# Performance work log

Measured on AMD Instinct MI355X. Metric: run time of the kernel, lower is better.

Reference implementation:

```python
import jax, jax.numpy as jnp
import numpy as np

N = 8192
C = 256


def setup_inputs() -> dict:
    key = jax.random.key(0)
    k_x, k_wr, k_br, k_wc, k_bc = jax.random.split(key, 5)
    scale = 1.0 / np.sqrt(C)
    return {
        "x": jax.random.normal(k_x, (N, C), dtype=jnp.float32),
        "w_reduce": jax.random.uniform(k_wr, (C, C), dtype=jnp.float32, minval=-scale, maxval=scale),
        "b_reduce": jax.random.uniform(k_br, (C,), dtype=jnp.float32, minval=-scale, maxval=scale),
        "w_contr": jax.random.uniform(k_wc, (1, C), dtype=jnp.float32, minval=-scale, maxval=scale),
        "b_contr": jax.random.uniform(k_bc, (1,), dtype=jnp.float32, minval=-scale, maxval=scale),
    }


def reference(x, w_reduce, b_reduce, w_contr, b_contr):
    # Original math: y_ij = reduce(x_i + x_j); z_ij = sigmoid(contr(y_ij));
    # out_i = mean_j y_ij * z_ij.
    # Since reduce/contr are affine, decompose without the [N,N,C] tensor:
    #   y_ij = r_i + r_j + b_reduce,        r = x @ Wr^T
    #   contr(y_ij) = s_i + s_j + c0,       s = r . wc, c0 = b_reduce . wc + bc
    n = x.shape[0]
    r = x @ w_reduce.T                                   # [N, C]
    wc = w_contr[0]                                      # [C]
    s = r @ wc                                           # [N]
    c0 = b_reduce @ wc + b_contr[0]                      # scalar
    Z = jax.nn.sigmoid(s[:, None] + s[None, :] + c0)     # [N, N] pairwise gate
    m = jnp.mean(Z, axis=1, keepdims=True)               # [N, 1]
    # mean_j (r_i + r_j + b) * z_ij = (r_i + b) * m_i + (Z @ r)_i / N
    out = (r + b_reduce) * m + (Z @ r) / n               # [N, C]
    return out
```

## Files before the change

### kernel.cpp

```cpp
#include <hip/hip_runtime.h>
#include <hip/hip_bf16.h>
#include <stdint.h>

#define NN 8192
#define CC 256
#define NSPLIT 8
#define JR (NN / NSPLIT)
#define NITER (JR / 32)

typedef float f32x4 __attribute__((ext_vector_type(4)));
typedef float f32x2 __attribute__((ext_vector_type(2)));
typedef short s16x8 __attribute__((ext_vector_type(8)));

#define LOG2E 1.4426950408889634f

#define OFF_WT  0
#define OFF_R   (OFF_WT + CC*CC)
#define OFF_S2  (OFF_R + NN*CC)
#define OFF_C0  (OFF_S2 + NN)
#define OFF_SS  (OFF_C0 + 16)
#define OFF_SP  (OFF_SS + NSPLIT*NN)
#define OFF_V   (OFF_SP + 4*NN)
#define OFF_RB  (OFF_V + (NSPLIT*NN*CC)/2)

__global__ __launch_bounds__(256) void k_prep(const float* __restrict__ w,
                                              const float* __restrict__ br,
                                              const float* __restrict__ wcv,
                                              const float* __restrict__ bc,
                                              float* __restrict__ ws) {
  int k = blockIdx.x, c = threadIdx.x;
  ws[OFF_WT + k * CC + c] = w[c * CC + k];
  if (blockIdx.x == 0 && threadIdx.x < 64) {
    int lane = threadIdx.x;
    f32x4 b4 = *(const f32x4*)&br[lane * 4];
    f32x4 w4 = *(const f32x4*)&wcv[lane * 4];
    float d = b4[0]*w4[0] + b4[1]*w4[1] + b4[2]*w4[2] + b4[3]*w4[3];
    #pragma unroll
    for (int m = 32; m >= 1; m >>= 1) d += __shfl_xor(d, m, 64);
    if (lane == 0) { ws[OFF_C0] = d + bc[0]; ws[OFF_C0 + 1] = (d + bc[0]) * LOG2E; }
  }
}

__global__ __launch_bounds__(256) void k_r(const float* __restrict__ x,
                                           const float* __restrict__ wcv,
                                           float* __restrict__ ws) {
  __shared__ float xs[64][260];
  int bi = blockIdx.x;
  int rowblk = bi >> 2, colblk = bi & 3;
  int tid = threadIdx.x;
  int i0 = rowblk * 64;
  for (int t = tid; t < 64 * 64; t += 256) {
    int rr = t >> 6, c4 = t & 63;
    *(f32x4*)&xs[rr][c4 * 4] = *(const f32x4*)&x[(i0 + rr) * CC + c4 * 4];
  }
  __syncthreads();
  int tx = tid & 15, ty = tid >> 4;
  int cbase = colblk * 64 + tx * 4;
  int r0 = ty * 4;
  float acc[4][4] = {};
  const float* wt = ws + OFF_WT;
  for (int k = 0; k < CC; k += 2) {
    f32x4 wv0 = *(const f32x4*)&wt[k * CC + cbase];
    f32x4 wv1 = *(const f32x4*)&wt[(k + 1) * CC + cbase];
    f32x2 xv[4];
    #pragma unroll
    for (int rr = 0; rr < 4; rr++) xv[rr] = *(const f32x2*)&xs[r0 + rr][k];
    #pragma unroll
    for (int rr = 0; rr < 4; rr++)
      #pragma unroll
      for (int cc = 0; cc < 4; cc++)
        acc[rr][cc] = fmaf(xv[rr][1], wv1[cc], fmaf(xv[rr][0], wv0[cc], acc[rr][cc]));
  }
  #pragma unroll
  for (int rr = 0; rr < 4; rr++) {
    f32x4 o = {acc[rr][0], acc[rr][1], acc[rr][2], acc[rr][3]};
    *(f32x4*)&ws[OFF_R + (size_t)(i0 + r0 + rr) * CC + cbase] = o;
  }
  unsigned long long* rb64 = (unsigned long long*)(ws + OFF_RB);
  int j0r = i0 + r0;
  #pragma unroll
  for (int cc = 0; cc < 4; cc++) {
    int c = cbase + cc;
    unsigned long long v = 0;
    #pragma unroll
    for (int rr = 0; rr < 4; rr++) {
      unsigned u = __float_as_uint(acc[rr][cc]);
      u = (u + 0x7fffu + ((u >> 16) & 1u)) >> 16;
      v |= (unsigned long long)u << (16 * rr);
    }
    int us = (((j0r >> 5) * 16 + (c >> 4)) * 64 + (((j0r >> 3) & 3) * 16 + (c & 15))) * 8 + (j0r & 7);
    rb64[us >> 2] = v;
  }
  f32x4 wc4 = *(const f32x4*)&wcv[cbase];
  float sd[4];
  #pragma unroll
  for (int rr = 0; rr < 4; rr++) {
    sd[rr] = acc[rr][0]*wc4[0] + acc[rr][1]*wc4[1] + acc[rr][2]*wc4[2] + acc[rr][3]*wc4[3];
    #pragma unroll
    for (int m = 1; m < 16; m <<= 1) sd[rr] += __shfl_xor(sd[rr], m, 64);
  }
  if (tx == 0) {
    #pragma unroll
    for (int rr = 0; rr < 4; rr++)
      ws[OFF_SP + colblk * NN + j0r + rr] = sd[rr];
  }
}

__global__ __launch_bounds__(256) void k_s2(float* __restrict__ ws) {
  int row = blockIdx.x * 256 + threadIdx.x;
  float s = ws[OFF_SP + row] + ws[OFF_SP + NN + row]
          + ws[OFF_SP + 2 * NN + row] + ws[OFF_SP + 3 * NN + row];
  ws[OFF_S2 + row] = s * LOG2E;
}


#define STAGE(BUF, IT) { \
  const char* gb_ = rbase + (size_t)(IT) * 16384 + w * 1024 + l * 16; \
  _Pragma("unroll") \
  for (int q_ = 0; q_ < 8; q_++) \
    __builtin_amdgcn_global_load_lds( \
      (const __attribute__((address_space(1))) void*)(gb_ + q_ * 2048), \
      (__attribute__((address_space(3))) void*)&ldsb[(BUF) * 16384 + w * 1024 + q_ * 2048 + l * 16], \
      16, 0, 0); }

#define WAITBAR0 { asm volatile("s_waitcnt vmcnt(0)" ::: "memory"); \
  __builtin_amdgcn_s_barrier(); \
  __builtin_amdgcn_sched_barrier(0); }

#define SB0 __builtin_amdgcn_sched_barrier(0);

#define SIGMOID(IT, AFA, AFB) { \
  f32x4 sj0_ = *(const f32x4*)&s2l[(IT) * 32 + g * 8]; \
  f32x4 sj1_ = *(const f32x4*)&s2l[(IT) * 32 + g * 8 + 4]; \
  _Pragma("unroll") \
  for (int t_ = 0; t_ < 8; t_++) { \
    float sj_ = (t_ < 4) ? sj0_[t_] : sj1_[t_ - 4]; \
    float eA_, eB_; \
    asm("v_exp_f32 %0, %1" : "=v"(eA_) : "v"(negaA - sj_)); \
    asm("v_exp_f32 %0, %1" : "=v"(eB_) : "v"(negaB - sj_)); \
    float zA_ = __builtin_amdgcn_rcpf(1.0f + eA_); \
    float zB_ = __builtin_amdgcn_rcpf(1.0f + eB_); \
    (AFA)[t_] = (short)(__float_as_uint(zA_) >> 16); \
    (AFB)[t_] = (short)(__float_as_uint(zB_) >> 16); } }

#define MFMA_PHASE(AFA, AFB, LP) { \
  _Pragma("unroll") \
  for (int ct_ = 0; ct_ < 16; ct_++) { \
    s16x8 bf_ = *(const s16x8*)((LP) + ct_ * 1024 + l * 16); \
    accA[ct_] = __builtin_amdgcn_mfma_f32_16x16x32_bf16(AFA, bf_, accA[ct_], 0, 0, 0); \
    accB[ct_] = __builtin_amdgcn_mfma_f32_16x16x32_bf16(AFB, bf_, accB[ct_], 0, 0, 0); } \
  acc1A = __builtin_amdgcn_mfma_f32_16x16x32_bf16(AFA, ones, acc1A, 0, 0, 0); \
  acc1B = __builtin_amdgcn_mfma_f32_16x16x32_bf16(AFB, ones, acc1B, 0, 0, 0); }

__global__ __launch_bounds__(128, 2) void k_main(float* __restrict__ ws) {
  __shared__ char ldsb[2 * 16384];
  __shared__ float s2l[1024];
  int blk = blockIdx.x;
  int rt = blk >> 3, h = blk & 7;
  int tid = threadIdx.x;
  int w = tid >> 6, l = tid & 63;
  int lr = l & 15, g = l >> 4;
  int iw = rt * 64 + w * 32;
  float c02 = ws[OFF_C0 + 1];
  float negaA = -(ws[OFF_S2 + iw + lr] + c02);
  float negaB = -(ws[OFF_S2 + iw + 16 + lr] + c02);

  const float* s2p = ws + OFF_S2 + h * JR;
  *(f32x4*)&s2l[tid * 4] = *(const f32x4*)(s2p + tid * 4);
  *(f32x4*)&s2l[(tid + 128) * 4] = *(const f32x4*)(s2p + (tid + 128) * 4);
  __syncthreads();

  f32x4 accA[16], accB[16], acc1A, acc1B;
  #pragma unroll
  for (int i = 0; i < 16; i++) { accA[i] = (f32x4)(0.f); accB[i] = (f32x4)(0.f); }
  acc1A = (f32x4)(0.f); acc1B = (f32x4)(0.f);
  s16x8 ones;
  #pragma unroll
  for (int t = 0; t < 8; t++) ones[t] = (short)0x3F80;

  const char* rbase = (const char*)(ws + OFF_RB) + (size_t)h * (JR * CC * 2);

  STAGE(0, 0);
  s16x8 afA, afB;
  #pragma unroll 1
  for (int J = 0; J < NITER; ++J) {
    WAITBAR0;
    if (J + 1 < NITER) STAGE((J + 1) & 1, J + 1);
    SB0;
    SIGMOID(J, afA, afB);
    MFMA_PHASE(afA, afB, ldsb + (J & 1) * 16384);
  }

  if (lr == 0) {
    #pragma unroll
    for (int q = 0; q < 4; q++) {
      ws[OFF_SS + h * NN + iw + g * 4 + q] = acc1A[q];
      ws[OFF_SS + h * NN + iw + 16 + g * 4 + q] = acc1B[q];
    }
  }
  unsigned short* Vb = (unsigned short*)(ws + OFF_V);
  size_t vbase = (size_t)h * (NN * CC);
  #pragma unroll
  for (int ct = 0; ct < 16; ct++) {
    #pragma unroll
    for (int q = 0; q < 4; q++) {
      unsigned uA = __float_as_uint(accA[ct][q]);
      uA = (uA + 0x7fffu + ((uA >> 16) & 1u)) >> 16;
      Vb[vbase + (size_t)(iw + g * 4 + q) * CC + ct * 16 + lr] = (unsigned short)uA;
      unsigned uB = __float_as_uint(accB[ct][q]);
      uB = (uB + 0x7fffu + ((uB >> 16) & 1u)) >> 16;
      Vb[vbase + (size_t)(iw + 16 + g * 4 + q) * CC + ct * 16 + lr] = (unsigned short)uB;
    }
  }
}

__global__ __launch_bounds__(256) void k_epi(const float* __restrict__ br,
                                             const float* __restrict__ ws,
                                             float* __restrict__ out) {
  int idx = blockIdx.x * 256 + threadIdx.x;
  int i = idx >> 5, c8 = (idx & 31) * 8;
  float S = 0.f;
  #pragma unroll
  for (int p = 0; p < NSPLIT; p++) S += ws[OFF_SS + p * NN + i];
  float m = S * (1.0f / NN);
  float v[8] = {};
  const unsigned short* Vb = (const unsigned short*)(ws + OFF_V);
  #pragma unroll
  for (int p = 0; p < NSPLIT; p++) {
    s16x8 pv = *(const s16x8*)&Vb[(size_t)p * (NN * CC) + (size_t)i * CC + c8];
    #pragma unroll
    for (int t = 0; t < 8; t++)
      v[t] += __uint_as_float(((unsigned)(unsigned short)pv[t]) << 16);
  }
  f32x4 r0 = *(const f32x4*)&ws[OFF_R + (size_t)i * CC + c8];
  f32x4 r1 = *(const f32x4*)&ws[OFF_R + (size_t)i * CC + c8 + 4];
  f32x4 b0 = *(const f32x4*)&br[c8];
  f32x4 b1 = *(const f32x4*)&br[c8 + 4];
  f32x4 o0, o1;
  #pragma unroll
  for (int t = 0; t < 4; t++) {
    o0[t] = (r0[t] + b0[t]) * m + v[t] * (1.0f / NN);
    o1[t] = (r1[t] + b1[t]) * m + v[t + 4] * (1.0f / NN);
  }
  *(f32x4*)&out[(size_t)i * CC + c8] = o0;
  *(f32x4*)&out[(size_t)i * CC + c8 + 4] = o1;
}

extern "C" void kernel_launch(void* const* d_in, const int* in_sizes, int n_in,
                              void* d_out, int out_size, void* d_ws, size_t ws_size,
                              hipStream_t stream) {
  const float* x  = (const float*)d_in[0];
  const float* w  = (const float*)d_in[1];
  const float* br = (const float*)d_in[2];
  const float* wc = (const float*)d_in[3];
  const float* bc = (const float*)d_in[4];
  float* ws = (float*)d_ws;
  float* out = (float*)d_out;
  (void)in_sizes; (void)n_in; (void)out_size; (void)ws_size;

  k_prep<<<256, 256, 0, stream>>>(w, br, wc, bc, ws);
  k_r<<<512, 256, 0, stream>>>(x, wc, ws);
  k_s2<<<32, 256, 0, stream>>>(ws);
  k_main<<<1024, 128, 0, stream>>>(ws);
  k_epi<<<1024, 256, 0, stream>>>(br, ws, out);
}
```

Baseline: 85.01 us.

## Widen k_main row tile to 64 rows per wave and sum gates in registers

Each wave now handles four 16-row fragments instead of two, so each B fragment loaded from LDS feeds four MFMAs. This halves the grid and the total global-to-LDS traffic of r. The row-sum of Z is now accumulated in fp32 registers with lane shuffles instead of through an extra MFMA against a ones vector, and bf16 packing uses v_cvt_pk_bf16_f32 (round-to-nearest) instead of truncation. The cost is double the accumulator registers (launch bounds drop to one block per SIMD) and fewer blocks, which lowers occupancy and latency hiding.

```diff
diff --git a/kernel.cpp b/kernel.cpp
--- a/kernel.cpp
+++ b/kernel.cpp
@@ -114,6 +114,8 @@
 }
 
 
+union U8 { s16x8 v; unsigned u[4]; };
+
 #define STAGE(BUF, IT) { \
   const char* gb_ = rbase + (size_t)(IT) * 16384 + w * 1024 + l * 16; \
   _Pragma("unroll") \
@@ -129,89 +131,100 @@
 
 #define SB0 __builtin_amdgcn_sched_barrier(0);
 
-#define SIGMOID(IT, AFA, AFB) { \
-  f32x4 sj0_ = *(const f32x4*)&s2l[(IT) * 32 + g * 8]; \
-  f32x4 sj1_ = *(const f32x4*)&s2l[(IT) * 32 + g * 8 + 4]; \
+#define SIG4(IT, AF) { \
+  f32x4 a0_ = *(const f32x4*)&s2l[(IT) * 32 + g * 8]; \
+  f32x4 a1_ = *(const f32x4*)&s2l[(IT) * 32 + g * 8 + 4]; \
   _Pragma("unroll") \
-  for (int t_ = 0; t_ < 8; t_++) { \
-    float sj_ = (t_ < 4) ? sj0_[t_] : sj1_[t_ - 4]; \
-    float eA_, eB_; \
-    asm("v_exp_f32 %0, %1" : "=v"(eA_) : "v"(negaA - sj_)); \
-    asm("v_exp_f32 %0, %1" : "=v"(eB_) : "v"(negaB - sj_)); \
-    float zA_ = __builtin_amdgcn_rcpf(1.0f + eA_); \
-    float zB_ = __builtin_amdgcn_rcpf(1.0f + eB_); \
-    (AFA)[t_] = (short)(__float_as_uint(zA_) >> 16); \
-    (AFB)[t_] = (short)(__float_as_uint(zB_) >> 16); } }
-
-#define MFMA_PHASE(AFA, AFB, LP) { \
+  for (int f_ = 0; f_ < 4; f_++) { \
+    float z_[8]; \
+    _Pragma("unroll") \
+    for (int t_ = 0; t_ < 8; t_++) { \
+      float sj_ = (t_ < 4) ? a0_[t_] : a1_[t_ - 4]; \
+      float e_; \
+      asm("v_exp_f32 %0, %1" : "=v"(e_) : "v"(nega[f_] - sj_)); \
+      float zz_ = __builtin_amdgcn_rcpf(1.0f + e_); \
+      ssum[f_] += zz_; \
+      z_[t_] = zz_; \
+    } \
+    U8 u8_; \
+    asm("v_cvt_pk_bf16_f32 %0, %1, %2" : "=v"(u8_.u[0]) : "v"(z_[0]), "v"(z_[1])); \
+    asm("v_cvt_pk_bf16_f32 %0, %1, %2" : "=v"(u8_.u[1]) : "v"(z_[2]), "v"(z_[3])); \
+    asm("v_cvt_pk_bf16_f32 %0, %1, %2" : "=v"(u8_.u[2]) : "v"(z_[4]), "v"(z_[5])); \
+    asm("v_cvt_pk_bf16_f32 %0, %1, %2" : "=v"(u8_.u[3]) : "v"(z_[6]), "v"(z_[7])); \
+    AF[f_] = u8_.v; \
+  } }
+
+#define MF4(AF, LP) { \
   _Pragma("unroll") \
   for (int ct_ = 0; ct_ < 16; ct_++) { \
     s16x8 bf_ = *(const s16x8*)((LP) + ct_ * 1024 + l * 16); \
-    accA[ct_] = __builtin_amdgcn_mfma_f32_16x16x32_bf16(AFA, bf_, accA[ct_], 0, 0, 0); \
-    accB[ct_] = __builtin_amdgcn_mfma_f32_16x16x32_bf16(AFB, bf_, accB[ct_], 0, 0, 0); } \
-  acc1A = __builtin_amdgcn_mfma_f32_16x16x32_bf16(AFA, ones, acc1A, 0, 0, 0); \
-  acc1B = __builtin_amdgcn_mfma_f32_16x16x32_bf16(AFB, ones, acc1B, 0, 0, 0); }
-
-__global__ __launch_bounds__(128, 2) void k_main(float* __restrict__ ws) {
+    _Pragma("unroll") \
+    for (int f_ = 0; f_ < 4; f_++) \
+      acc[f_][ct_] = __builtin_amdgcn_mfma_f32_16x16x32_bf16(AF[f_], bf_, acc[f_][ct_], 0, 0, 0); \
+  } }
+
+__global__ __launch_bounds__(128, 1) void k_main(float* __restrict__ ws) {
   __shared__ char ldsb[2 * 16384];
-  __shared__ float s2l[1024];
+  __shared__ float s2l[JR];
   int blk = blockIdx.x;
   int rt = blk >> 3, h = blk & 7;
   int tid = threadIdx.x;
   int w = tid >> 6, l = tid & 63;
   int lr = l & 15, g = l >> 4;
-  int iw = rt * 64 + w * 32;
+  int iw = rt * 128 + w * 64;
   float c02 = ws[OFF_C0 + 1];
-  float negaA = -(ws[OFF_S2 + iw + lr] + c02);
-  float negaB = -(ws[OFF_S2 + iw + 16 + lr] + c02);
+  float nega[4];
+  #pragma unroll
+  for (int f = 0; f < 4; f++)
+    nega[f] = -(ws[OFF_S2 + iw + f * 16 + lr] + c02);
 
   const float* s2p = ws + OFF_S2 + h * JR;
   *(f32x4*)&s2l[tid * 4] = *(const f32x4*)(s2p + tid * 4);
   *(f32x4*)&s2l[(tid + 128) * 4] = *(const f32x4*)(s2p + (tid + 128) * 4);
   __syncthreads();
 
-  f32x4 accA[16], accB[16], acc1A, acc1B;
-  #pragma unroll
-  for (int i = 0; i < 16; i++) { accA[i] = (f32x4)(0.f); accB[i] = (f32x4)(0.f); }
-  acc1A = (f32x4)(0.f); acc1B = (f32x4)(0.f);
-  s16x8 ones;
-  #pragma unroll
-  for (int t = 0; t < 8; t++) ones[t] = (short)0x3F80;
+  f32x4 acc[4][16];
+  #pragma unroll
+  for (int f = 0; f < 4; f++)
+    #pragma unroll
+    for (int ct = 0; ct < 16; ct++) acc[f][ct] = (f32x4)(0.f);
+  float ssum[4] = {0.f, 0.f, 0.f, 0.f};
 
   const char* rbase = (const char*)(ws + OFF_RB) + (size_t)h * (JR * CC * 2);
 
   STAGE(0, 0);
-  s16x8 afA, afB;
+  s16x8 af[4];
   #pragma unroll 1
   for (int J = 0; J < NITER; ++J) {
     WAITBAR0;
     if (J + 1 < NITER) STAGE((J + 1) & 1, J + 1);
     SB0;
-    SIGMOID(J, afA, afB);
-    MFMA_PHASE(afA, afB, ldsb + (J & 1) * 16384);
-  }
-
-  if (lr == 0) {
-    #pragma unroll
-    for (int q = 0; q < 4; q++) {
-      ws[OFF_SS + h * NN + iw + g * 4 + q] = acc1A[q];
-      ws[OFF_SS + h * NN + iw + 16 + g * 4 + q] = acc1B[q];
-    }
+    SIG4(J, af);
+    MF4(af, ldsb + (J & 1) * 16384);
+  }
+
+  #pragma unroll
+  for (int f = 0; f < 4; f++) {
+    ssum[f] += __shfl_xor(ssum[f], 16, 64);
+    ssum[f] += __shfl_xor(ssum[f], 32, 64);
+  }
+  if (l < 16) {
+    #pragma unroll
+    for (int f = 0; f < 4; f++)
+      ws[OFF_SS + h * NN + iw + f * 16 + lr] = ssum[f];
   }
   unsigned short* Vb = (unsigned short*)(ws + OFF_V);
   size_t vbase = (size_t)h * (NN * CC);
   #pragma unroll
-  for (int ct = 0; ct < 16; ct++) {
-    #pragma unroll
-    for (int q = 0; q < 4; q++) {
-      unsigned uA = __float_as_uint(accA[ct][q]);
-      uA = (uA + 0x7fffu + ((uA >> 16) & 1u)) >> 16;
-      Vb[vbase + (size_t)(iw + g * 4 + q) * CC + ct * 16 + lr] = (unsigned short)uA;
-      unsigned uB = __float_as_uint(accB[ct][q]);
-      uB = (uB + 0x7fffu + ((uB >> 16) & 1u)) >> 16;
-      Vb[vbase + (size_t)(iw + 16 + g * 4 + q) * CC + ct * 16 + lr] = (unsigned short)uB;
-    }
-  }
+  for (int f = 0; f < 4; f++)
+    #pragma unroll
+    for (int ct = 0; ct < 16; ct++)
+      #pragma unroll
+      for (int q = 0; q < 4; q++) {
+        unsigned u = __float_as_uint(acc[f][ct][q]);
+        u = (u + 0x7fffu + ((u >> 16) & 1u)) >> 16;
+        Vb[vbase + (size_t)(iw + f * 16 + g * 4 + q) * CC + ct * 16 + lr] = (unsigned short)u;
+      }
 }
 
 __global__ __launch_bounds__(256) void k_epi(const float* __restrict__ br,
@@ -261,6 +274,6 @@
   k_prep<<<256, 256, 0, stream>>>(w, br, wc, bc, ws);
   k_r<<<512, 256, 0, stream>>>(x, wc, ws);
   k_s2<<<32, 256, 0, stream>>>(ws);
-  k_main<<<1024, 128, 0, stream>>>(ws);
+  k_main<<<512, 128, 0, stream>>>(ws);
   k_epi<<<1024, 256, 0, stream>>>(br, ws, out);
 }
```

After: 98.82 us. 16.2% more time.
